# Performance work log

Measured on AMD Instinct MI355X. Metric: run time of the kernel, lower is better.

## Reference

```python
import jax, jax.numpy as jnp
import numpy as np

D_MODEL = 768
HEADS = 12
D_K = D_MODEL // HEADS
NEG = -1e9


def setup_inputs() -> dict:
    key = jax.random.key(0)
    ks = jax.random.split(key, 7)
    B, S, D = 4, 2048, D_MODEL
    scale = 1.0 / np.sqrt(D)
    q = jax.random.normal(ks[0], (B, S, D), dtype=jnp.float32)
    k = jax.random.normal(ks[1], (B, S, D), dtype=jnp.float32)
    v = jax.random.normal(ks[2], (B, S, D), dtype=jnp.float32)
    # causal mask, broadcastable over batch and heads; mask==0 -> -1e9
    mask = jnp.tril(jnp.ones((1, 1, S, S), dtype=jnp.int32))
    W_q = jax.random.normal(ks[3], (D, D), dtype=jnp.float32) * scale
    W_k = jax.random.normal(ks[4], (D, D), dtype=jnp.float32) * scale
    W_v = jax.random.normal(ks[5], (D, D), dtype=jnp.float32) * scale
    W_o = jax.random.normal(ks[6], (D, D), dtype=jnp.float32) * scale
    return {"q": q, "k": k, "v": v, "mask": mask,
            "W_q": W_q, "W_k": W_k, "W_v": W_v, "W_o": W_o}


def reference(q, k, v, mask, W_q, W_k, W_v, W_o):
    B, S, D = q.shape
    # nn.Linear(bias=False): y = x @ W.T
    query = (q @ W_q.T).reshape(B, S, HEADS, D_K).transpose(0, 2, 1, 3)  # [B,H,S,dk]
    key_ = (k @ W_k.T).reshape(B, S, HEADS, D_K).transpose(0, 2, 1, 3)
    value = (v @ W_v.T).reshape(B, S, HEADS, D_K).transpose(0, 2, 1, 3)
    scores = jnp.einsum('bhqd,bhkd->bhqk', query, key_) / jnp.sqrt(
        jnp.asarray(D_K, dtype=query.dtype))
    scores = jnp.where(mask == 0, jnp.asarray(NEG, dtype=scores.dtype), scores)
    attn = jax.nn.softmax(scores, axis=-1)
    # dropout rate = 0.0 (inference / eval mode): identity
    x = jnp.einsum('bhqk,bhkd->bhqd', attn, value)  # [B,H,S,dk]
    x = x.transpose(0, 2, 1, 3).reshape(B, S, D)
    return x @ W_o.T
```

## Files before the change

kernel.cpp:

```cpp
#include <hip/hip_runtime.h>


typedef _Float16 f16x8 __attribute__((ext_vector_type(8)));
typedef _Float16 f16x4 __attribute__((ext_vector_type(4)));
typedef float floatx4 __attribute__((ext_vector_type(4)));

#define MFMA16(a, b, c) __builtin_amdgcn_mfma_f32_16x16x32_f16((a), (b), (c), 0, 0, 0)

static constexpr int B_ = 4;
static constexpr int S_ = 2048;
static constexpr int D_ = 768;
static constexpr int H_ = 12;
static constexpr int DK = 64;

__device__ __forceinline__ f16x8 cvt8(float4 a, float4 b) {
  f16x8 h;
  h[0] = (_Float16)a.x; h[1] = (_Float16)a.y;
  h[2] = (_Float16)a.z; h[3] = (_Float16)a.w;
  h[4] = (_Float16)b.x; h[5] = (_Float16)b.y;
  h[6] = (_Float16)b.z; h[7] = (_Float16)b.w;
  return h;
}

__device__ __forceinline__ void dma16(const _Float16* g, _Float16* l) {
  __builtin_amdgcn_global_load_lds(
      (const __attribute__((address_space(1))) unsigned int*)g,
      (__attribute__((address_space(3))) unsigned int*)l, 16, 0, 0);
}

struct CvtArgs {
  const float* src[7];
  _Float16* dst[7];
  int end[7];
  int nseg;
};

__global__ __launch_bounds__(256) void cvt_f32_f16(CvtArgs a) {
  int b = blockIdx.x;
  int s = 0;
  while (s < a.nseg - 1 && b >= a.end[s]) ++s;
  int local = b - (s ? a.end[s - 1] : 0);
  const int tid = threadIdx.x;
  const float4* p = (const float4*)(a.src[s] + (size_t)local * 2048) + tid * 2;
  float4 x0 = p[0], x1 = p[1];
  *(f16x8*)(a.dst[s] + (size_t)local * 2048 + tid * 8) = cvt8(x0, x1);
}

static constexpr int PAN = 128 * 32;

struct QkvPtrs {
  const void* a[3];
  const void* w[3];
};

template <int MODE, bool SCALE>
__device__ __forceinline__ void gemm_core64(const _Float16* __restrict__ A,
                                            const _Float16* __restrict__ Bm,
                                            void* __restrict__ Cv,
                                            _Float16* As, _Float16* Bs,
                                            int m0, int n0, int N, int K) {
  const int tid = threadIdx.x;
  const int wave = tid >> 6, lane = tid & 63;
  const int l15 = lane & 15, quad = lane >> 4;
  const int wm = (wave >> 1) * 64, wn = (wave & 1) * 64;
  const int lr = lane >> 2;
  const int lc = (lane & 3) * 8;
  const int wb = wave * 16;

  floatx4 acc[4][4] = {};

  for (int k0 = 0; k0 < K; k0 += 64) {
    {
      const _Float16* g = A + (size_t)(m0 + wb + lr) * K + k0 + lc;
      dma16(g, As + wb * 32);
      dma16(g + 32, As + PAN + wb * 32);
      const _Float16* g2 = g + (size_t)64 * K;
      dma16(g2, As + (64 + wb) * 32);
      dma16(g2 + 32, As + PAN + (64 + wb) * 32);
    }
    {
      const _Float16* g = Bm + (size_t)(n0 + wb + lr) * K + k0 + lc;
      dma16(g, Bs + wb * 32);
      dma16(g + 32, Bs + PAN + wb * 32);
      const _Float16* g2 = g + (size_t)64 * K;
      dma16(g2, Bs + (64 + wb) * 32);
      dma16(g2 + 32, Bs + PAN + (64 + wb) * 32);
    }
    __syncthreads();

#pragma unroll
    for (int p = 0; p < 2; ++p) {
      f16x8 af[4], bf[4];
#pragma unroll
      for (int t = 0; t < 4; ++t)
        af[t] = *(const f16x8*)(As + p * PAN + (wm + t * 16 + l15) * 32 +
                                quad * 8);
#pragma unroll
      for (int t = 0; t < 4; ++t)
        bf[t] = *(const f16x8*)(Bs + p * PAN + (wn + t * 16 + l15) * 32 +
                                quad * 8);
#pragma unroll
      for (int mt = 0; mt < 4; ++mt)
#pragma unroll
        for (int nt = 0; nt < 4; ++nt)
          acc[mt][nt] = MFMA16(af[mt], bf[nt], acc[mt][nt]);
    }
    __syncthreads();
  }

  if constexpr (MODE == 2) {
#pragma unroll
    for (int mt = 0; mt < 4; ++mt)
#pragma unroll
      for (int nt = 0; nt < 4; ++nt) {
        int row = m0 + wm + mt * 16 + quad * 4;
        int col = n0 + wn + nt * 16 + l15;
        int b = row >> 11, s = row & 2047;
        int h = col >> 6, d = col & 63;
        f16x4 v4;
#pragma unroll
        for (int r = 0; r < 4; ++r) v4[r] = (_Float16)acc[mt][nt][r];
        *(f16x4*)((_Float16*)Cv + ((size_t)(b * H_ + h) * DK + d) * S_ + s) =
            v4;
      }
  } else {
#pragma unroll
    for (int mt = 0; mt < 4; ++mt)
#pragma unroll
      for (int nt = 0; nt < 4; ++nt)
#pragma unroll
        for (int r = 0; r < 4; ++r) {
          int row = m0 + wm + mt * 16 + quad * 4 + r;
          int col = n0 + wn + nt * 16 + l15;
          float val = acc[mt][nt][r];
          if constexpr (SCALE) val *= 0.125f;
          if constexpr (MODE == 0) {
            ((float*)Cv)[(size_t)row * N + col] = val;
          } else {
            int b = row >> 11, s = row & 2047;
            int h = col >> 6, d = col & 63;
            ((_Float16*)Cv)[((size_t)(b * H_ + h) * S_ + s) * DK + d] =
                (_Float16)val;
          }
        }
  }
}

__global__ __launch_bounds__(256) void qkv_gemm64(QkvPtrs P, _Float16* Qh,
                                                  _Float16* Kh, _Float16* Vt) {
  __shared__ _Float16 As[2 * PAN];
  __shared__ _Float16 Bs[2 * PAN];
  const int z = blockIdx.z;
  const int m0 = blockIdx.y * 128, n0 = blockIdx.x * 128;
  if (z == 0) {
    gemm_core64<1, true>((const _Float16*)P.a[0], (const _Float16*)P.w[0], Qh,
                         As, Bs, m0, n0, D_, D_);
  } else if (z == 1) {
    gemm_core64<1, false>((const _Float16*)P.a[1], (const _Float16*)P.w[1], Kh,
                          As, Bs, m0, n0, D_, D_);
  } else {
    gemm_core64<2, false>((const _Float16*)P.a[2], (const _Float16*)P.w[2], Vt,
                          As, Bs, m0, n0, D_, D_);
  }
}

static constexpr int PAN_A = 64 * 32;
static constexpr int PAN_B = 128 * 32;

__global__ __launch_bounds__(256) void gemm_o64(const _Float16* __restrict__ A,
                                                const _Float16* __restrict__ W,
                                                float* __restrict__ C) {
  __shared__ _Float16 As[2 * PAN_A];
  __shared__ _Float16 Bs[2 * PAN_B];
  constexpr int K = 768, N = 768;

  const int tid = threadIdx.x;
  const int wave = tid >> 6, lane = tid & 63;
  const int l15 = lane & 15, quad = lane >> 4;
  const int wm = (wave >> 1) * 32, wn = (wave & 1) * 64;
  const int m0 = blockIdx.y * 64, n0 = blockIdx.x * 128;
  const int lr = lane >> 2, lc = (lane & 3) * 8;

  floatx4 acc[2][4] = {};

  for (int k0 = 0; k0 < K; k0 += 64) {
#pragma unroll
    for (int p = 0; p < 2; ++p) {
      const _Float16* g =
          A + (size_t)(m0 + wave * 16 + lr) * K + k0 + p * 32 + lc;
      dma16(g, As + p * PAN_A + wave * 16 * 32);
    }
#pragma unroll
    for (int p = 0; p < 2; ++p)
#pragma unroll
      for (int q = 0; q < 2; ++q) {
        const _Float16* g =
            W + (size_t)(n0 + wave * 32 + q * 16 + lr) * K + k0 + p * 32 + lc;
        dma16(g, Bs + p * PAN_B + (wave * 32 + q * 16) * 32);
      }
    __syncthreads();

#pragma unroll
    for (int p = 0; p < 2; ++p) {
      f16x8 af[2], bf[4];
#pragma unroll
      for (int t = 0; t < 2; ++t)
        af[t] = *(const f16x8*)(As + p * PAN_A + (wm + t * 16 + l15) * 32 +
                                quad * 8);
#pragma unroll
      for (int t = 0; t < 4; ++t)
        bf[t] = *(const f16x8*)(Bs + p * PAN_B + (wn + t * 16 + l15) * 32 +
                                quad * 8);
#pragma unroll
      for (int mt = 0; mt < 2; ++mt)
#pragma unroll
        for (int nt = 0; nt < 4; ++nt)
          acc[mt][nt] = MFMA16(af[mt], bf[nt], acc[mt][nt]);
    }
    __syncthreads();
  }

#pragma unroll
  for (int mt = 0; mt < 2; ++mt)
#pragma unroll
    for (int nt = 0; nt < 4; ++nt)
#pragma unroll
      for (int r = 0; r < 4; ++r) {
        int row = m0 + wm + mt * 16 + quad * 4 + r;
        int col = n0 + wn + nt * 16 + l15;
        C[(size_t)row * N + col] = acc[mt][nt][r];
      }
}

__global__ __launch_bounds__(256, 3) void flash_attn(
    const _Float16* __restrict__ Qh, const _Float16* __restrict__ Kh,
    const _Float16* __restrict__ Vt, _Float16* __restrict__ Oh) {
  __shared__ _Float16 Ks[64 * 72];
  __shared__ _Float16 Vts[64 * 72];
  __shared__ _Float16 Ps[4][16 * 36];

  const int tid = threadIdx.x;
  const int wave = tid >> 6, lane = tid & 63;
  const int l15 = lane & 15, quad = lane >> 4;

  const int linear = blockIdx.x + gridDim.x * blockIdx.y;
  const int xcd = linear & 7;
  const int seq = linear >> 3;
  const int bh = xcd * 6 + (seq >> 3);
  const int x = seq & 7;
  const int b = bh / H_, h = bh % H_;
  const size_t base = (size_t)bh * S_ * DK;
  const size_t basev = (size_t)bh * DK * S_;

  const int srow = tid >> 2;
  const int sc0 = (tid & 3) * 16;

  for (int c = 0; c < 2; ++c) {
    const int qt = c ? x : 15 - x;
    const int q0 = qt * 128;
    const int jmax = 2 * qt + 1;

    f16x8 qf[2][2];
#pragma unroll
    for (int mt = 0; mt < 2; ++mt) {
      int qrow = q0 + mt * 64 + wave * 16 + l15;
      qf[mt][0] = *(const f16x8*)(Qh + base + (size_t)qrow * DK + quad * 8);
      qf[mt][1] =
          *(const f16x8*)(Qh + base + (size_t)qrow * DK + 32 + quad * 8);
    }

    floatx4 o_acc[2][4] = {};
    float plsum[2][4] = {};

    const _Float16* ks = Kh + base + (size_t)srow * DK + sc0;
    const _Float16* vs = Vt + basev + (size_t)srow * S_ + sc0;
    f16x8 pk0 = *(const f16x8*)ks;
    f16x8 pk1 = *(const f16x8*)(ks + 8);
    f16x8 pv0 = *(const f16x8*)vs;
    f16x8 pv1 = *(const f16x8*)(vs + 8);

    for (int j = 0; j <= jmax; ++j) {
      const int j0 = j * 64;
      __syncthreads();
      *(f16x8*)(Ks + srow * 72 + sc0) = pk0;
      *(f16x8*)(Ks + srow * 72 + sc0 + 8) = pk1;
      *(f16x8*)(Vts + srow * 72 + sc0) = pv0;
      *(f16x8*)(Vts + srow * 72 + sc0 + 8) = pv1;
      __syncthreads();

      if (j < jmax) {
        const _Float16* kn =
            Kh + base + (size_t)((j + 1) * 64 + srow) * DK + sc0;
        const _Float16* vn =
            Vt + basev + (size_t)srow * S_ + (j + 1) * 64 + sc0;
        pk0 = *(const f16x8*)kn;
        pk1 = *(const f16x8*)(kn + 8);
        pv0 = *(const f16x8*)vn;
        pv1 = *(const f16x8*)(vn + 8);
      }

      const int rb0 = q0 + wave * 16;
      const int rb1 = q0 + 64 + wave * 16;
      const bool a0 = (j0 <= rb0 + 15);
      const bool a1 = (j0 <= rb1 + 15);

      floatx4 s_acc[2][4] = {};
#pragma unroll
      for (int t = 0; t < 4; ++t) {
        f16x8 kf0 = *(const f16x8*)(Ks + (t * 16 + l15) * 72 + quad * 8);
        f16x8 kf1 = *(const f16x8*)(Ks + (t * 16 + l15) * 72 + 32 + quad * 8);
        if (a0) {
          s_acc[0][t] = MFMA16(qf[0][0], kf0, s_acc[0][t]);
          s_acc[0][t] = MFMA16(qf[0][1], kf1, s_acc[0][t]);
        }
        if (a1) {
          s_acc[1][t] = MFMA16(qf[1][0], kf0, s_acc[1][t]);
          s_acc[1][t] = MFMA16(qf[1][1], kf1, s_acc[1][t]);
        }
      }

      f16x8 pf[2][2];
#pragma unroll
      for (int mt = 0; mt < 2; ++mt) {
        const bool act = mt ? a1 : a0;
        if (!act) continue;
        const int rbase = mt ? rb1 : rb0;
        const bool need_mask = (j0 + 63 > rbase);
        float p[4][4];
#pragma unroll
        for (int t = 0; t < 4; ++t)
#pragma unroll
          for (int r = 0; r < 4; ++r) {
            float s = s_acc[mt][t][r];
            if (need_mask) {
              int rg = rbase + quad * 4 + r;
              int cg = j0 + t * 16 + l15;
              if (cg > rg) s = -1e30f;
            }
            float e = __expf(s);
            p[t][r] = e;
            plsum[mt][r] += e;
          }
#pragma unroll
        for (int t = 0; t < 2; ++t)
#pragma unroll
          for (int r = 0; r < 4; ++r)
            Ps[wave][(quad * 4 + r) * 36 + t * 16 + l15] = (_Float16)p[t][r];
        pf[mt][0] = *(const f16x8*)(Ps[wave] + l15 * 36 + quad * 8);
#pragma unroll
        for (int t = 2; t < 4; ++t)
#pragma unroll
          for (int r = 0; r < 4; ++r)
            Ps[wave][(quad * 4 + r) * 36 + (t - 2) * 16 + l15] =
                (_Float16)p[t][r];
        pf[mt][1] = *(const f16x8*)(Ps[wave] + l15 * 36 + quad * 8);
      }

#pragma unroll
      for (int t = 0; t < 4; ++t) {
        f16x8 vf0 = *(const f16x8*)(Vts + (t * 16 + l15) * 72 + quad * 8);
        f16x8 vf1 = *(const f16x8*)(Vts + (t * 16 + l15) * 72 + 32 + quad * 8);
        if (a0) {
          o_acc[0][t] = MFMA16(pf[0][0], vf0, o_acc[0][t]);
          o_acc[0][t] = MFMA16(pf[0][1], vf1, o_acc[0][t]);
        }
        if (a1) {
          o_acc[1][t] = MFMA16(pf[1][0], vf0, o_acc[1][t]);
          o_acc[1][t] = MFMA16(pf[1][1], vf1, o_acc[1][t]);
        }
      }
    }

#pragma unroll
    for (int mt = 0; mt < 2; ++mt)
#pragma unroll
      for (int r = 0; r < 4; ++r) {
        float l = plsum[mt][r];
        l += __shfl_xor(l, 1);
        l += __shfl_xor(l, 2);
        l += __shfl_xor(l, 4);
        l += __shfl_xor(l, 8);
        float inv = 1.0f / l;
        int row = q0 + mt * 64 + wave * 16 + quad * 4 + r;
#pragma unroll
        for (int t = 0; t < 4; ++t) {
          float val = o_acc[mt][t][r] * inv;
          Oh[((size_t)(b * S_ + row)) * D_ + h * DK + t * 16 + l15] =
              (_Float16)val;
        }
      }
  }
}

template <int MODE, bool SCALE>
__global__ __launch_bounds__(256) void gemm128(const float* __restrict__ Av,
                                               const float* __restrict__ Bv,
                                               void* __restrict__ Cv, int M,
                                               int N, int K) {
  __shared__ _Float16 As[128 * 40];
  __shared__ _Float16 Bs[128 * 40];

  const int tid = threadIdx.x;
  const int wave = tid >> 6, lane = tid & 63;
  const int l15 = lane & 15, quad = lane >> 4;
  const int wm = (wave >> 1) * 64, wn = (wave & 1) * 64;
  const int m0 = blockIdx.y * 128, n0 = blockIdx.x * 128;
  const int srow = tid >> 1, scol = (tid & 1) * 16;

  floatx4 acc[4][4] = {};

  for (int k0 = 0; k0 < K; k0 += 32) {
    {
      const float4* p =
          (const float4*)(Av + (size_t)(m0 + srow) * K + k0 + scol);
      float4 x0 = p[0], x1 = p[1], x2 = p[2], x3 = p[3];
      *(f16x8*)(As + srow * 40 + scol) = cvt8(x0, x1);
      *(f16x8*)(As + srow * 40 + scol + 8) = cvt8(x2, x3);
    }
    {
      const float4* p =
          (const float4*)(Bv + (size_t)(n0 + srow) * K + k0 + scol);
      float4 x0 = p[0], x1 = p[1], x2 = p[2], x3 = p[3];
      *(f16x8*)(Bs + srow * 40 + scol) = cvt8(x0, x1);
      *(f16x8*)(Bs + srow * 40 + scol + 8) = cvt8(x2, x3);
    }
    __syncthreads();

    f16x8 af[4], bf[4];
#pragma unroll
    for (int t = 0; t < 4; ++t)
      af[t] = *(const f16x8*)(As + (wm + t * 16 + l15) * 40 + quad * 8);
#pragma unroll
    for (int t = 0; t < 4; ++t)
      bf[t] = *(const f16x8*)(Bs + (wn + t * 16 + l15) * 40 + quad * 8);
#pragma unroll
    for (int mt = 0; mt < 4; ++mt)
#pragma unroll
      for (int nt = 0; nt < 4; ++nt)
        acc[mt][nt] = MFMA16(af[mt], bf[nt], acc[mt][nt]);
    __syncthreads();
  }

#pragma unroll
  for (int mt = 0; mt < 4; ++mt)
#pragma unroll
    for (int nt = 0; nt < 4; ++nt)
#pragma unroll
      for (int r = 0; r < 4; ++r) {
        int row = m0 + wm + mt * 16 + quad * 4 + r;
        int col = n0 + wn + nt * 16 + l15;
        float val = acc[mt][nt][r];
        if constexpr (SCALE) val *= 0.125f;
        if constexpr (MODE == 0) {
          ((float*)Cv)[(size_t)row * N + col] = val;
        } else if constexpr (MODE == 1) {
          int b = row >> 11, s = row & 2047;
          int h = col >> 6, d = col & 63;
          ((_Float16*)Cv)[((size_t)(b * H_ + h) * S_ + s) * DK + d] =
              (_Float16)val;
        } else {
          int b = col >> 11, s = col & 2047;
          int h = row >> 6, d = row & 63;
          ((_Float16*)Cv)[((size_t)(b * H_ + h) * DK + d) * S_ + s] =
              (_Float16)val;
        }
      }
}

__global__ __launch_bounds__(256) void gemm_out_f32w(
    const _Float16* __restrict__ A, const float* __restrict__ Bv,
    float* __restrict__ C) {
  __shared__ _Float16 As[128 * 40];
  __shared__ _Float16 Bs[128 * 40];
  constexpr int K = 768, N = 768;

  const int tid = threadIdx.x;
  const int wave = tid >> 6, lane = tid & 63;
  const int l15 = lane & 15, quad = lane >> 4;
  const int wm = (wave >> 1) * 64, wn = (wave & 1) * 64;
  const int m0 = blockIdx.y * 128, n0 = blockIdx.x * 128;
  const int srow = tid >> 1, scol = (tid & 1) * 16;

  floatx4 acc[4][4] = {};

  for (int k0 = 0; k0 < K; k0 += 32) {
    {
      const f16x8* p = (const f16x8*)(A + (size_t)(m0 + srow) * K + k0 + scol);
      *(f16x8*)(As + srow * 40 + scol) = p[0];
      *(f16x8*)(As + srow * 40 + scol + 8) = p[1];
    }
    {
      const float4* p =
          (const float4*)(Bv + (size_t)(n0 + srow) * K + k0 + scol);
      float4 x0 = p[0], x1 = p[1], x2 = p[2], x3 = p[3];
      *(f16x8*)(Bs + srow * 40 + scol) = cvt8(x0, x1);
      *(f16x8*)(Bs + srow * 40 + scol + 8) = cvt8(x2, x3);
    }
    __syncthreads();

    f16x8 af[4], bf[4];
#pragma unroll
    for (int t = 0; t < 4; ++t)
      af[t] = *(const f16x8*)(As + (wm + t * 16 + l15) * 40 + quad * 8);
#pragma unroll
    for (int t = 0; t < 4; ++t)
      bf[t] = *(const f16x8*)(Bs + (wn + t * 16 + l15) * 40 + quad * 8);
#pragma unroll
    for (int mt = 0; mt < 4; ++mt)
#pragma unroll
      for (int nt = 0; nt < 4; ++nt)
        acc[mt][nt] = MFMA16(af[mt], bf[nt], acc[mt][nt]);
    __syncthreads();
  }

#pragma unroll
  for (int mt = 0; mt < 4; ++mt)
#pragma unroll
    for (int nt = 0; nt < 4; ++nt)
#pragma unroll
      for (int r = 0; r < 4; ++r) {
        int row = m0 + wm + mt * 16 + quad * 4 + r;
        int col = n0 + wn + nt * 16 + l15;
        C[(size_t)row * N + col] = acc[mt][nt][r];
      }
}

extern "C" void kernel_launch(void* const* d_in, const int* in_sizes, int n_in,
                              void* d_out, int out_size, void* d_ws,
                              size_t ws_size, hipStream_t stream) {
  const float* q = (const float*)d_in[0];
  const float* k = (const float*)d_in[1];
  const float* v = (const float*)d_in[2];
  const float* Wq = (const float*)d_in[4];
  const float* Wk = (const float*)d_in[5];
  const float* Wv = (const float*)d_in[6];
  const float* Wo = (const float*)d_in[7];
  float* out = (float*)d_out;

  const size_t E = (size_t)B_ * H_ * S_ * DK;
  const size_t EW = (size_t)D_ * D_;
  _Float16* Qh = (_Float16*)d_ws;
  _Float16* Kh = Qh + E;
  _Float16* Vt = Kh + E;
  _Float16* Oh = Vt + E;

  const int M = B_ * S_;
  dim3 blk(256);
  dim3 qg(D_ / 128, M / 128, 3);
  dim3 og(D_ / 128, M / 64);
  dim3 pg(D_ / 128, M / 128);
  dim3 fg(8, B_ * H_);

  const size_t need_full = (7 * E + 4 * EW) * 2;

  if (ws_size >= need_full) {
    _Float16* qf = Oh + E;
    _Float16* kf = qf + E;
    _Float16* vf = kf + E;
    _Float16* wqf = vf + E;
    _Float16* wkf = wqf + EW;
    _Float16* wvf = wkf + EW;
    _Float16* wof = wvf + EW;
    CvtArgs ca;
    ca.src[0] = q;  ca.dst[0] = qf;
    ca.src[1] = k;  ca.dst[1] = kf;
    ca.src[2] = v;  ca.dst[2] = vf;
    ca.src[3] = Wq; ca.dst[3] = wqf;
    ca.src[4] = Wk; ca.dst[4] = wkf;
    ca.src[5] = Wv; ca.dst[5] = wvf;
    ca.src[6] = Wo; ca.dst[6] = wof;
    int ends[7] = {3072, 6144, 9216, 9504, 9792, 10080, 10368};
    for (int i = 0; i < 7; ++i) ca.end[i] = ends[i];
    ca.nseg = 7;
    cvt_f32_f16<<<10368, blk, 0, stream>>>(ca);
    QkvPtrs P;
    P.a[0] = qf; P.a[1] = kf; P.a[2] = vf;
    P.w[0] = wqf; P.w[1] = wkf; P.w[2] = wvf;
    qkv_gemm64<<<qg, blk, 0, stream>>>(P, Qh, Kh, Vt);
    flash_attn<<<fg, blk, 0, stream>>>(Qh, Kh, Vt, Oh);
    gemm_o64<<<og, blk, 0, stream>>>(Oh, wof, out);
  } else {
    gemm128<1, true><<<pg, blk, 0, stream>>>(q, Wq, Qh, M, D_, D_);
    gemm128<1, false><<<pg, blk, 0, stream>>>(k, Wk, Kh, M, D_, D_);
    gemm128<2, false><<<dim3(M / 128, D_ / 128), blk, 0, stream>>>(
        Wv, v, Vt, D_, M, D_);
    flash_attn<<<fg, blk, 0, stream>>>(Qh, Kh, Vt, Oh);
    gemm_out_f32w<<<pg, blk, 0, stream>>>(Oh, Wo, out);
  }
}
```

Measured before the change: 280.8 us.

## Shrink flash-attention query tile to 64 rows and remap GEMM blocks per XCD

Flash attention now processes 64-row query tiles instead of 128, doubling the grid and pairing tiles 31-x and x for causal load balance. Each wave handles one 16-row M-tile, which lowers register use so occupancy can be raised to 4 blocks per SIMD set via launch bounds. The QKV and output GEMMs remap block indices so that neighbouring M panels land on the same XCD, improving L2 reuse of the A rows. The trade-off is that K/V tiles are loaded from global memory twice as often per query row, and there are more loop iterations with barriers.

```diff
diff --git a/kernel.cpp b/kernel.cpp
--- a/kernel.cpp
+++ b/kernel.cpp
@@ -150,8 +150,15 @@
                                                   _Float16* Kh, _Float16* Vt) {
   __shared__ _Float16 As[2 * PAN];
   __shared__ _Float16 Bs[2 * PAN];
-  const int z = blockIdx.z;
-  const int m0 = blockIdx.y * 128, n0 = blockIdx.x * 128;
+  const int linear =
+      blockIdx.x + gridDim.x * (blockIdx.y + gridDim.y * blockIdx.z);
+  const int xcd = linear & 7;
+  const int idx = linear >> 3;
+  const int z = idx / 48;
+  const int r = idx % 48;
+  const int mp = xcd * 8 + (r / 6);
+  const int n = r % 6;
+  const int m0 = mp * 128, n0 = n * 128;
   if (z == 0) {
     gemm_core64<1, true>((const _Float16*)P.a[0], (const _Float16*)P.w[0], Qh,
                          As, Bs, m0, n0, D_, D_);
@@ -174,11 +181,17 @@
   __shared__ _Float16 Bs[2 * PAN_B];
   constexpr int K = 768, N = 768;
 
+  const int linear = blockIdx.x + gridDim.x * blockIdx.y;
+  const int xcd = linear & 7;
+  const int idx = linear >> 3;
+  const int mp = xcd * 16 + idx / 6;
+  const int n = idx % 6;
+  const int m0 = mp * 64, n0 = n * 128;
+
   const int tid = threadIdx.x;
   const int wave = tid >> 6, lane = tid & 63;
   const int l15 = lane & 15, quad = lane >> 4;
   const int wm = (wave >> 1) * 32, wn = (wave & 1) * 64;
-  const int m0 = blockIdx.y * 64, n0 = blockIdx.x * 128;
   const int lr = lane >> 2, lc = (lane & 3) * 8;
 
   floatx4 acc[2][4] = {};
@@ -232,7 +245,7 @@
       }
 }
 
-__global__ __launch_bounds__(256, 3) void flash_attn(
+__global__ __launch_bounds__(256, 4) void flash_attn(
     const _Float16* __restrict__ Qh, const _Float16* __restrict__ Kh,
     const _Float16* __restrict__ Vt, _Float16* __restrict__ Oh) {
   __shared__ _Float16 Ks[64 * 72];
@@ -246,8 +259,8 @@
   const int linear = blockIdx.x + gridDim.x * blockIdx.y;
   const int xcd = linear & 7;
   const int seq = linear >> 3;
-  const int bh = xcd * 6 + (seq >> 3);
-  const int x = seq & 7;
+  const int bh = xcd * 6 + (seq >> 4);
+  const int xp = seq & 15;
   const int b = bh / H_, h = bh % H_;
   const size_t base = (size_t)bh * S_ * DK;
   const size_t basev = (size_t)bh * DK * S_;
@@ -256,21 +269,14 @@
   const int sc0 = (tid & 3) * 16;
 
   for (int c = 0; c < 2; ++c) {
-    const int qt = c ? x : 15 - x;
-    const int q0 = qt * 128;
-    const int jmax = 2 * qt + 1;
-
-    f16x8 qf[2][2];
-#pragma unroll
-    for (int mt = 0; mt < 2; ++mt) {
-      int qrow = q0 + mt * 64 + wave * 16 + l15;
-      qf[mt][0] = *(const f16x8*)(Qh + base + (size_t)qrow * DK + quad * 8);
-      qf[mt][1] =
-          *(const f16x8*)(Qh + base + (size_t)qrow * DK + 32 + quad * 8);
-    }
-
-    floatx4 o_acc[2][4] = {};
-    float plsum[2][4] = {};
+    const int qt = c ? xp : 31 - xp;
+    const int q0 = qt * 64;
+    const int qrow = q0 + wave * 16 + l15;
+    f16x8 qf0 = *(const f16x8*)(Qh + base + (size_t)qrow * DK + quad * 8);
+    f16x8 qf1 = *(const f16x8*)(Qh + base + (size_t)qrow * DK + 32 + quad * 8);
+
+    floatx4 o_acc[4] = {};
+    float plsum[4] = {0.f, 0.f, 0.f, 0.f};
 
     const _Float16* ks = Kh + base + (size_t)srow * DK + sc0;
     const _Float16* vs = Vt + basev + (size_t)srow * S_ + sc0;
@@ -279,8 +285,7 @@
     f16x8 pv0 = *(const f16x8*)vs;
     f16x8 pv1 = *(const f16x8*)(vs + 8);
 
-    for (int j = 0; j <= jmax; ++j) {
-      const int j0 = j * 64;
+    for (int j = 0; j <= qt; ++j) {
       __syncthreads();
       *(f16x8*)(Ks + srow * 72 + sc0) = pk0;
       *(f16x8*)(Ks + srow * 72 + sc0 + 8) = pk1;
@@ -288,7 +293,7 @@
       *(f16x8*)(Vts + srow * 72 + sc0 + 8) = pv1;
       __syncthreads();
 
-      if (j < jmax) {
+      if (j < qt) {
         const _Float16* kn =
             Kh + base + (size_t)((j + 1) * 64 + srow) * DK + sc0;
         const _Float16* vn =
@@ -299,96 +304,74 @@
         pv1 = *(const f16x8*)(vn + 8);
       }
 
-      const int rb0 = q0 + wave * 16;
-      const int rb1 = q0 + 64 + wave * 16;
-      const bool a0 = (j0 <= rb0 + 15);
-      const bool a1 = (j0 <= rb1 + 15);
-
-      floatx4 s_acc[2][4] = {};
+      floatx4 s_acc[4] = {};
 #pragma unroll
       for (int t = 0; t < 4; ++t) {
         f16x8 kf0 = *(const f16x8*)(Ks + (t * 16 + l15) * 72 + quad * 8);
         f16x8 kf1 = *(const f16x8*)(Ks + (t * 16 + l15) * 72 + 32 + quad * 8);
-        if (a0) {
-          s_acc[0][t] = MFMA16(qf[0][0], kf0, s_acc[0][t]);
-          s_acc[0][t] = MFMA16(qf[0][1], kf1, s_acc[0][t]);
+        s_acc[t] = MFMA16(qf0, kf0, s_acc[t]);
+        s_acc[t] = MFMA16(qf1, kf1, s_acc[t]);
+      }
+
+      const bool diag = (j == qt);
+      const int j0 = j * 64;
+      float p[4][4];
+#pragma unroll
+      for (int t = 0; t < 4; ++t)
+#pragma unroll
+        for (int r = 0; r < 4; ++r) {
+          float s = s_acc[t][r];
+          if (diag) {
+            int rg = q0 + wave * 16 + quad * 4 + r;
+            int cg = j0 + t * 16 + l15;
+            if (cg > rg) s = -1e30f;
+          }
+          float e = __expf(s);
+          p[t][r] = e;
+          plsum[r] += e;
         }
-        if (a1) {
-          s_acc[1][t] = MFMA16(qf[1][0], kf0, s_acc[1][t]);
-          s_acc[1][t] = MFMA16(qf[1][1], kf1, s_acc[1][t]);
-        }
-      }
-
-      f16x8 pf[2][2];
-#pragma unroll
-      for (int mt = 0; mt < 2; ++mt) {
-        const bool act = mt ? a1 : a0;
-        if (!act) continue;
-        const int rbase = mt ? rb1 : rb0;
-        const bool need_mask = (j0 + 63 > rbase);
-        float p[4][4];
-#pragma unroll
-        for (int t = 0; t < 4; ++t)
-#pragma unroll
-          for (int r = 0; r < 4; ++r) {
-            float s = s_acc[mt][t][r];
-            if (need_mask) {
-              int rg = rbase + quad * 4 + r;
-              int cg = j0 + t * 16 + l15;
-              if (cg > rg) s = -1e30f;
-            }
-            float e = __expf(s);
-            p[t][r] = e;
-            plsum[mt][r] += e;
-          }
-#pragma unroll
-        for (int t = 0; t < 2; ++t)
-#pragma unroll
-          for (int r = 0; r < 4; ++r)
-            Ps[wave][(quad * 4 + r) * 36 + t * 16 + l15] = (_Float16)p[t][r];
-        pf[mt][0] = *(const f16x8*)(Ps[wave] + l15 * 36 + quad * 8);
-#pragma unroll
-        for (int t = 2; t < 4; ++t)
-#pragma unroll
-          for (int r = 0; r < 4; ++r)
-            Ps[wave][(quad * 4 + r) * 36 + (t - 2) * 16 + l15] =
-                (_Float16)p[t][r];
-        pf[mt][1] = *(const f16x8*)(Ps[wave] + l15 * 36 + quad * 8);
-      }
-
+
+#pragma unroll
+      for (int t = 0; t < 2; ++t)
+#pragma unroll
+        for (int r = 0; r < 4; ++r)
+          Ps[wave][(quad * 4 + r) * 36 + t * 16 + l15] = (_Float16)p[t][r];
+      f16x8 pf0 = *(const f16x8*)(Ps[wave] + l15 * 36 + quad * 8);
 #pragma unroll
       for (int t = 0; t < 4; ++t) {
         f16x8 vf0 = *(const f16x8*)(Vts + (t * 16 + l15) * 72 + quad * 8);
+        o_acc[t] = MFMA16(pf0, vf0, o_acc[t]);
+      }
+#pragma unroll
+      for (int t = 2; t < 4; ++t)
+#pragma unroll
+        for (int r = 0; r < 4; ++r)
+          Ps[wave][(quad * 4 + r) * 36 + (t - 2) * 16 + l15] =
+              (_Float16)p[t][r];
+      f16x8 pf1 = *(const f16x8*)(Ps[wave] + l15 * 36 + quad * 8);
+#pragma unroll
+      for (int t = 0; t < 4; ++t) {
         f16x8 vf1 = *(const f16x8*)(Vts + (t * 16 + l15) * 72 + 32 + quad * 8);
-        if (a0) {
-          o_acc[0][t] = MFMA16(pf[0][0], vf0, o_acc[0][t]);
-          o_acc[0][t] = MFMA16(pf[0][1], vf1, o_acc[0][t]);
-        }
-        if (a1) {
-          o_acc[1][t] = MFMA16(pf[1][0], vf0, o_acc[1][t]);
-          o_acc[1][t] = MFMA16(pf[1][1], vf1, o_acc[1][t]);
-        }
-      }
-    }
-
-#pragma unroll
-    for (int mt = 0; mt < 2; ++mt)
-#pragma unroll
-      for (int r = 0; r < 4; ++r) {
-        float l = plsum[mt][r];
-        l += __shfl_xor(l, 1);
-        l += __shfl_xor(l, 2);
-        l += __shfl_xor(l, 4);
-        l += __shfl_xor(l, 8);
-        float inv = 1.0f / l;
-        int row = q0 + mt * 64 + wave * 16 + quad * 4 + r;
-#pragma unroll
-        for (int t = 0; t < 4; ++t) {
-          float val = o_acc[mt][t][r] * inv;
-          Oh[((size_t)(b * S_ + row)) * D_ + h * DK + t * 16 + l15] =
-              (_Float16)val;
-        }
-      }
+        o_acc[t] = MFMA16(pf1, vf1, o_acc[t]);
+      }
+    }
+
+#pragma unroll
+    for (int r = 0; r < 4; ++r) {
+      float l = plsum[r];
+      l += __shfl_xor(l, 1);
+      l += __shfl_xor(l, 2);
+      l += __shfl_xor(l, 4);
+      l += __shfl_xor(l, 8);
+      float inv = 1.0f / l;
+      int row = q0 + wave * 16 + quad * 4 + r;
+#pragma unroll
+      for (int t = 0; t < 4; ++t) {
+        float val = o_acc[t][r] * inv;
+        Oh[((size_t)(b * S_ + row)) * D_ + h * DK + t * 16 + l15] =
+            (_Float16)val;
+      }
+    }
   }
 }
 
@@ -549,7 +532,7 @@
   dim3 qg(D_ / 128, M / 128, 3);
   dim3 og(D_ / 128, M / 64);
   dim3 pg(D_ / 128, M / 128);
-  dim3 fg(8, B_ * H_);
+  dim3 fg(16, B_ * H_);
 
   const size_t need_full = (7 * E + 4 * EW) * 2;
 
```

Measured after the change: 245.5 us. -12.6%, faster.
